# Kernel optimization log

Measured on AMD Instinct MI355X. Metric: run time of the kernel, lower is better.

Reference implementation:

```python
import jax, jax.numpy as jnp
import numpy as np

B, L, D_MODEL = 2, 1024, 512
N_LAYERS = 4
D_INNER = 2 * D_MODEL          # expand=2
D_STATE = 16
D_CONV = 4
DT_RANK = D_MODEL // 16        # ceil(512/16)=32
EPS = 1e-5


def layernorm(x, w, b):
    m = jnp.mean(x, axis=-1, keepdims=True)
    v = jnp.var(x, axis=-1, keepdims=True)
    return (x - m) * jax.lax.rsqrt(v + EPS) * w + b


def selective_scan(u, delta, A, Bm, Cm, Dp):
    # u, delta: [b,l,d]; Bm, Cm: [b,l,n]; A: [d,n]; Dp: [d]
    def step(h, inp):
        dt_t, b_t, c_t, u_t = inp            # [b,d],[b,n],[b,n],[b,d]
        dA = jnp.exp(dt_t[:, :, None] * A)   # [b,d,n]
        h = dA * h + (dt_t * u_t)[:, :, None] * b_t[:, None, :]
        y = jnp.einsum('bdn,bn->bd', h, c_t)
        return h, y

    b, l, d = u.shape
    n = A.shape[1]
    h0 = jnp.zeros((b, d, n), u.dtype)
    xs = (jnp.swapaxes(delta, 0, 1), jnp.swapaxes(Bm, 0, 1),
          jnp.swapaxes(Cm, 0, 1), jnp.swapaxes(u, 0, 1))
    _, ys = jax.lax.scan(step, h0, xs)       # ys: [l,b,d]
    return jnp.swapaxes(ys, 0, 1) + u * Dp


def mamba(x, in_w, conv_w, conv_b, xp_w, dtp_w, dtp_b, A_log, Dp, out_w):
    # x: [b,l,D_MODEL]
    xz = x @ in_w.T                          # [b,l,2*d_inner]
    xc, z = jnp.split(xz, 2, axis=-1)
    xc = jnp.swapaxes(xc, 1, 2)              # [b,d_inner,l]
    xc = jax.lax.conv_general_dilated(
        xc, conv_w[:, None, :], (1,), [(D_CONV - 1, 0)],
        feature_group_count=D_INNER,
        dimension_numbers=('NCH', 'OIH', 'NCH')) + conv_b[None, :, None]
    xc = jax.nn.silu(jnp.swapaxes(xc, 1, 2))  # [b,l,d_inner]
    x_dbl = xc @ xp_w.T                       # [b,l,dt_rank+2n]
    dt = x_dbl[..., :DT_RANK]
    Bm = x_dbl[..., DT_RANK:DT_RANK + D_STATE]
    Cm = x_dbl[..., DT_RANK + D_STATE:]
    dt = jax.nn.softplus(dt @ dtp_w.T + dtp_b)
    A = -jnp.exp(A_log)
    y = selective_scan(xc, dt, A, Bm, Cm, Dp)
    y = y * jax.nn.silu(z)
    return y @ out_w.T


def forward(x, in_proj_w, conv_w, conv_b, x_proj_w, dt_proj_w, dt_proj_b,
            A_log, D_param, out_proj_w, ln_w, ln_b, fnorm_w, fnorm_b):
    residual = None
    for i in range(in_proj_w.shape[0]):
        residual = x if residual is None else x + residual
        xn = layernorm(x, ln_w[i], ln_b[i])  # norm of incoming x (as in torch src)
        h1 = mamba(xn, in_proj_w[i, 0], conv_w[i, 0], conv_b[i, 0],
                   x_proj_w[i, 0], dt_proj_w[i, 0], dt_proj_b[i, 0],
                   A_log[i, 0], D_param[i, 0], out_proj_w[i, 0])
        h2 = mamba(jnp.flip(xn, axis=1), in_proj_w[i, 1], conv_w[i, 1],
                   conv_b[i, 1], x_proj_w[i, 1], dt_proj_w[i, 1],
                   dt_proj_b[i, 1], A_log[i, 1], D_param[i, 1],
                   out_proj_w[i, 1])
        x = h1 + h2                           # bi_add: NOT flipped back, faithful
    x = x + residual
    return layernorm(x, fnorm_w, fnorm_b)


def setup_inputs() -> dict:
    key = jax.random.key(0)
    ks = jax.random.split(key, 8)
    P2 = (N_LAYERS, 2)
    inp = {}
    inp['x'] = jax.random.normal(ks[0], (B, L, D_MODEL), jnp.float32)
    inp['in_proj_w'] = jax.random.normal(ks[1], P2 + (2 * D_INNER, D_MODEL), jnp.float32) * 0.02
    inp['conv_w'] = jax.random.normal(ks[2], P2 + (D_INNER, D_CONV), jnp.float32) * 0.1
    inp['conv_b'] = jnp.zeros(P2 + (D_INNER,), jnp.float32)
    inp['x_proj_w'] = jax.random.normal(ks[3], P2 + (DT_RANK + 2 * D_STATE, D_INNER), jnp.float32) * 0.02
    inp['dt_proj_w'] = jax.random.normal(ks[4], P2 + (D_INNER, DT_RANK), jnp.float32) * (DT_RANK ** -0.5)
    inp['dt_proj_b'] = jnp.full(P2 + (D_INNER,), float(np.log(np.expm1(0.01))), jnp.float32)
    inp['A_log'] = jnp.broadcast_to(jnp.log(jnp.arange(1, D_STATE + 1, dtype=jnp.float32)), P2 + (D_INNER, D_STATE)).copy()
    inp['D_param'] = jnp.ones(P2 + (D_INNER,), jnp.float32)
    inp['out_proj_w'] = jax.random.normal(ks[5], P2 + (D_MODEL, D_INNER), jnp.float32) * 0.02
    inp['ln_w'] = jnp.ones((N_LAYERS, D_MODEL), jnp.float32)
    inp['ln_b'] = jnp.zeros((N_LAYERS, D_MODEL), jnp.float32)
    inp['fnorm_w'] = jnp.ones((D_MODEL,), jnp.float32)
    inp['fnorm_b'] = jnp.zeros((D_MODEL,), jnp.float32)
    return inp


def reference(x, in_proj_w, conv_w, conv_b, x_proj_w, dt_proj_w, dt_proj_b,
              A_log, D_param, out_proj_w, ln_w, ln_b, fnorm_w, fnorm_b):
    return forward(x, in_proj_w, conv_w, conv_b, x_proj_w, dt_proj_w,
                   dt_proj_b, A_log, D_param, out_proj_w, ln_w, ln_b,
                   fnorm_w, fnorm_b)
```

## Files before the change

### kernel.cpp

```cpp
#include <hip/hip_runtime.h>
#include <hip/hip_bf16.h>
#include <type_traits>

#define B_   2
#define L_   1024
#define DM   512
#define DI   1024
#define DS   16
#define DTR  32
#define ROWS (B_*L_)
#define NCH  32
#define CHUNK (L_/NCH)

#define PO_CW    0
#define PO_CB    32768
#define PO_XPW   40960
#define PO_DTW   565248
#define PO_DTB   827392
#define PO_ALOG  835584
#define PO_DP    966656
#define PO_LNW   974848
#define PO_LNB   976896
#define PO_FNW   978944
#define PO_FNB   979456
#define PO_END   979968

#define N_WIN    (4*2097152)
#define N_WOUT   (4*1048576)
#define N_X      1048576

typedef __bf16 bf16x8 __attribute__((ext_vector_type(8)));
typedef float  f32x4  __attribute__((ext_vector_type(4)));
using bf16 = __hip_bfloat16;

__device__ __forceinline__ bf16x8 ld8(const bf16* p){
    return *reinterpret_cast<const bf16x8*>(p);
}
__device__ __forceinline__ float b2f(bf16 v){ return __bfloat162float(v); }

__device__ __forceinline__ unsigned pkbf2(float a, float b){
    bf16 ha = __float2bfloat16(a), hb = __float2bfloat16(b);
    unsigned short ua = *(unsigned short*)&ha, ub = *(unsigned short*)&hb;
    return (unsigned)ua | ((unsigned)ub << 16);
}
__device__ __forceinline__ float unpk_lo(unsigned v){
    unsigned x = v << 16; return __builtin_bit_cast(float, x);
}
__device__ __forceinline__ float unpk_hi(unsigned v){
    unsigned x = v & 0xffff0000u; return __builtin_bit_cast(float, x);
}

__device__ __forceinline__ void async_cp16(const void* g, void* s){
    __builtin_amdgcn_global_load_lds(
        (const __attribute__((address_space(1))) unsigned int*)g,
        (__attribute__((address_space(3))) unsigned int*)s, 16, 0, 0);
}

__global__ void detect_kernel(const void* Dp_raw, int* flag){
    *flag = (*(const unsigned int*)Dp_raw == 0x3F800000u) ? 1 : 0;
}

__device__ __forceinline__ bf16 cvload(const void* s, long o, int f){
    return f ? __float2bfloat16(((const float*)s)[o]) : ((const bf16*)s)[o];
}

__global__ void megacvt_kernel(const void* cw, const void* cb, const void* xpw,
                               const void* dtw, const void* dtb, const void* al,
                               const void* dp, const void* lnw, const void* lnb,
                               const void* fnw, const void* fnb,
                               const void* inw, const void* outw, const void* xin,
                               bf16* PP, bf16* WIN, bf16* WOUT,
                               float* X, float* R, const int* flag){
    long i = (long)blockIdx.x*256 + threadIdx.x;
    int f = *flag;
    if (i < PO_END){
        const void* s; long o;
        if      (i < PO_CB)   { s = cw;  o = i; }
        else if (i < PO_XPW)  { s = cb;  o = i - PO_CB; }
        else if (i < PO_DTW)  { s = xpw; o = i - PO_XPW; }
        else if (i < PO_DTB)  { s = dtw; o = i - PO_DTW; }
        else if (i < PO_ALOG) { s = dtb; o = i - PO_DTB; }
        else if (i < PO_DP)   { s = al;  o = i - PO_ALOG; }
        else if (i < PO_LNW)  { s = dp;  o = i - PO_DP; }
        else if (i < PO_LNB)  { s = lnw; o = i - PO_LNW; }
        else if (i < PO_FNW)  { s = lnb; o = i - PO_LNB; }
        else if (i < PO_FNB)  { s = fnw; o = i - PO_FNW; }
        else                  { s = fnb; o = i - PO_FNB; }
        PP[i] = cvload(s, o, f);
        return;
    }
    i -= PO_END;
    if (i < N_WIN){ WIN[i] = cvload(inw, i, f); return; }
    i -= N_WIN;
    if (i < N_WOUT){
        long l = i >> 20, r = i & 1048575;
        long n = r >> 11, dir = (r >> 10) & 1, d = r & 1023;
        WOUT[i] = cvload(outw, ((l*2 + dir)*512 + n)*1024 + d, f);
        return;
    }
    i -= N_WOUT;
    if (i < N_X){
        X[i] = f ? ((const float*)xin)[i] : b2f(((const bf16*)xin)[i]);
        R[i] = 0.f;
    }
}

__global__ void ln_kernel(const float* __restrict__ P, int nparts,
                          float* __restrict__ R,
                          const bf16* __restrict__ w, const bf16* __restrict__ b,
                          void* __restrict__ out, int mode, const int* flag){
    int row = blockIdx.x, lane = threadIdx.x;
    size_t base = (size_t)row*DM + lane*8;
    float v[8];
    *(float4*)&v[0] = *(const float4*)(P+base);
    *(float4*)&v[4] = *(const float4*)(P+base+4);
    for (int k=1; k<nparts; ++k){
        float4 a0 = *(const float4*)(P + (size_t)k*1048576 + base);
        float4 a1 = *(const float4*)(P + (size_t)k*1048576 + base + 4);
        v[0]+=a0.x; v[1]+=a0.y; v[2]+=a0.z; v[3]+=a0.w;
        v[4]+=a1.x; v[5]+=a1.y; v[6]+=a1.z; v[7]+=a1.w;
    }
    if (mode == 0){
        float4 r0 = *(const float4*)(R+base);
        float4 r1 = *(const float4*)(R+base+4);
        r0.x += v[0]; r0.y += v[1]; r0.z += v[2]; r0.w += v[3];
        r1.x += v[4]; r1.y += v[5]; r1.z += v[6]; r1.w += v[7];
        *(float4*)(R+base)   = r0;
        *(float4*)(R+base+4) = r1;
    } else {
        float4 r0 = *(const float4*)(R+base);
        float4 r1 = *(const float4*)(R+base+4);
        v[0]+=r0.x; v[1]+=r0.y; v[2]+=r0.z; v[3]+=r0.w;
        v[4]+=r1.x; v[5]+=r1.y; v[6]+=r1.z; v[7]+=r1.w;
    }
    float s=0.f, sq=0.f;
    #pragma unroll
    for (int j=0;j<8;++j){ s += v[j]; sq += v[j]*v[j]; }
    #pragma unroll
    for (int off=32; off>=1; off>>=1){
        s  += __shfl_xor(s,  off, 64);
        sq += __shfl_xor(sq, off, 64);
    }
    float mean = s*(1.f/DM);
    float var  = sq*(1.f/DM) - mean*mean;
    float rs   = rsqrtf(var + 1e-5f);
    bf16x8 wv = ld8(w + lane*8), bv = ld8(b + lane*8);
    float res[8];
    #pragma unroll
    for (int j=0;j<8;++j)
        res[j] = (v[j]-mean)*rs*(float)wv[j] + (float)bv[j];
    if (mode == 1 && *flag){
        float* of = (float*)out;
        *(float4*)(of+base)   = make_float4(res[0],res[1],res[2],res[3]);
        *(float4*)(of+base+4) = make_float4(res[4],res[5],res[6],res[7]);
    } else {
        union { bf16 h[8]; uint4 u; } o;
        #pragma unroll
        for (int j=0;j<8;++j) o.h[j] = __float2bfloat16(res[j]);
        *(uint4*)((bf16*)out + base) = o.u;
    }
}

template<int WM, int WN, int SK, typename CT>
__global__ __launch_bounds__(WM*WN*64)
void gemm_lds(const bf16* __restrict__ A, const bf16* __restrict__ W,
              CT* __restrict__ C, int K, int lda, int ldw, int ldc,
              int selTiles, long wSel){
    constexpr int BM = WM*64, BN = WN*64, T = WM*WN*64;
    constexpr int RA = (BM*4)/T, RB = (BN*4)/T;
    __shared__ __align__(16) bf16 sA[BM*32];
    __shared__ __align__(16) bf16 sB[BN*32];
    int tid = threadIdx.x;
    int mtile = blockIdx.y, ntile = blockIdx.x;
    if (mtile >= selTiles) W += wSel;
    int m0 = mtile*BM, n0 = ntile*BN;
    int kPer = K/SK, kBeg = blockIdx.z*kPer, kEnd = kBeg + kPer;
    if (SK > 1)
        C += (size_t)blockIdx.z * (size_t)(gridDim.y*BM) * (size_t)(gridDim.x*BN);
    int wave = tid>>6, lane = tid&63, quad = lane>>4, r = lane&15;
    int wrow = wave / WN, wcol = wave % WN;
    const bf16* Abase = A + (size_t)m0*lda;
    const bf16* Wbase = W + (size_t)n0*ldw;
    f32x4 acc[4][4] = {};
    for (int k0 = kBeg; k0 < kEnd; k0 += 32){
        #pragma unroll
        for (int rr=0; rr<RA; ++rr){
            int q = rr*T + tid;
            async_cp16(Abase + (size_t)(q>>2)*lda + k0 + (q&3)*8, &sA[q*8]);
        }
        #pragma unroll
        for (int rr=0; rr<RB; ++rr){
            int q = rr*T + tid;
            async_cp16(Wbase + (size_t)(q>>2)*ldw + k0 + (q&3)*8, &sB[q*8]);
        }
        __syncthreads();
        bf16x8 af[4], bw[4];
        #pragma unroll
        for (int mt=0; mt<4; ++mt)
            af[mt] = *(const bf16x8*)&sA[(wrow*64 + mt*16 + r)*32 + quad*8];
        #pragma unroll
        for (int nt=0; nt<4; ++nt)
            bw[nt] = *(const bf16x8*)&sB[(wcol*64 + nt*16 + r)*32 + quad*8];
        #pragma unroll
        for (int mt=0; mt<4; ++mt)
            #pragma unroll
            for (int nt=0; nt<4; ++nt)
                acc[mt][nt] = __builtin_amdgcn_mfma_f32_16x16x32_bf16(
                    af[mt], bw[nt], acc[mt][nt], 0,0,0);
        __syncthreads();
    }
    #pragma unroll
    for (int mt=0; mt<4; ++mt){
        #pragma unroll
        for (int nt=0; nt<4; ++nt){
            int col = n0 + wcol*64 + nt*16 + r;
            #pragma unroll
            for (int ri=0; ri<4; ++ri){
                int row = m0 + wrow*64 + mt*16 + quad*4 + ri;
                size_t idx = (size_t)row*ldc + col;
                if constexpr (std::is_same<CT, bf16>::value)
                    C[idx] = __float2bfloat16(acc[mt][nt][ri]);
                else
                    C[idx] = acc[mt][nt][ri];
            }
        }
    }
}

__global__ void reduce_xd(const float* __restrict__ P, float* __restrict__ XD){
    int i = blockIdx.x*256 + threadIdx.x;
    float s = 0.f;
    #pragma unroll
    for (int k=0;k<8;++k) s += P[k*262144 + i];
    int j = i & 63, grow = i >> 6, dir = grow >> 11, row = grow & 2047;
    XD[row*128 + dir*64 + j] = s;
}

__global__ void conv_kernel(const bf16* __restrict__ XZ, const bf16* __restrict__ cw,
                            const bf16* __restrict__ cb, const bf16* __restrict__ Dp,
                            bf16* __restrict__ XC, unsigned* __restrict__ GU){
    int id  = blockIdx.x*256 + threadIdx.x;
    int d   = id & (DI-1);
    int t   = (id >> 10) & (L_-1);
    int b   = (id >> 20) & 1;
    int dir = id >> 21;
    float wv[4];
    #pragma unroll
    for (int k=0;k<4;++k) wv[k] = b2f(cw[((size_t)dir*DI + d)*4 + k]);
    float acc = b2f(cb[dir*DI + d]);
    #pragma unroll
    for (int k=0;k<4;++k){
        int tau = t - 3 + k;
        if (tau >= 0){
            int sig = dir ? (L_-1-tau) : tau;
            acc += wv[k] * b2f(XZ[((size_t)(b*L_ + sig))*4096 + dir*2048 + d]);
        }
    }
    float u = acc * (1.f/(1.f + __expf(-acc)));
    size_t idx = ((size_t)dir*ROWS + (size_t)b*L_ + t)*DI + d;
    XC[idx] = __float2bfloat16(u);
    int sig3 = dir ? (L_-1-t) : t;
    float zv = b2f(XZ[((size_t)(b*L_ + sig3))*4096 + dir*2048 + 1024 + d]);
    float g  = zv*(1.f/(1.f + __expf(-zv)));
    float Dv = b2f(Dp[dir*DI + d]);
    GU[idx] = pkbf2(g, u*Dv*g);
}

__global__ void dtproj_kernel(const float* __restrict__ XD, const bf16* __restrict__ dtw,
                              const bf16* __restrict__ dtb, const bf16* __restrict__ XC,
                              unsigned* __restrict__ DTW){
    int id  = blockIdx.x*256 + threadIdx.x;
    int d   = id & (DI-1);
    int row = (id >> 10) & (ROWS-1);
    int dir = id >> 21;
    const float* xr = XD + (size_t)row*128 + dir*64;
    const bf16*  wp = dtw + ((size_t)dir*DI + d)*DTR;
    float acc = b2f(dtb[dir*DI + d]);
    #pragma unroll
    for (int kk=0;kk<4;++kk){
        bf16x8 wv = ld8(wp + kk*8);
        #pragma unroll
        for (int j=0;j<8;++j) acc += xr[kk*8+j]*(float)wv[j];
    }
    float sp = acc > 20.f ? acc : log1pf(__expf(acc));
    size_t idx = ((size_t)dir*ROWS + row)*DI + d;
    float u = b2f(XC[idx]);
    DTW[idx] = pkbf2(sp, sp*u);
}

template<int PHASE>
__global__ __launch_bounds__(256)
void scan_phase(const unsigned* __restrict__ DTW, const unsigned* __restrict__ GU,
                const float* __restrict__ XD, const bf16* __restrict__ Al,
                float* __restrict__ SP, float* __restrict__ SH,
                bf16* __restrict__ Y){
    int dirb = blockIdx.z, dir = dirb >> 1, b = dirb & 1;
    int c    = blockIdx.y;
    int d0   = blockIdx.x*128;
    int tid  = threadIdx.x;
    int dl   = tid >> 1, nh = tid & 1;
    int d    = d0 + dl;

    __shared__ __align__(16) unsigned sDTW[CHUNK*128];
    __shared__ __align__(16) float    sBC[CHUNK][32];
    __shared__ __align__(16) unsigned sGU[(PHASE==3)?CHUNK*128:4];

    const unsigned* DTWb = DTW + ((size_t)dir*ROWS + b*L_ + c*CHUNK)*DI + d0;
    #pragma unroll
    for (int it=0; it<4; ++it){
        int q = it*256 + tid;
        int t = q >> 5, c4 = q & 31;
        async_cp16(DTWb + (size_t)t*DI + c4*4, &sDTW[q*4]);
    }
    if (PHASE == 3){
        const unsigned* GUb = GU + ((size_t)dir*ROWS + b*L_ + c*CHUNK)*DI + d0;
        #pragma unroll
        for (int it=0; it<4; ++it){
            int q = it*256 + tid;
            int t = q >> 5, c4 = q & 31;
            async_cp16(GUb + (size_t)t*DI + c4*4, &sGU[q*4]);
        }
    }
    {
        int t = tid >> 3, j = tid & 7;
        async_cp16(XD + ((size_t)(b*L_) + c*CHUNK + t)*128 + dir*64 + 32 + j*4,
                   &sBC[t][j*4]);
    }

    float An[8];
    {
        const bf16* ap = Al + ((size_t)dir*DI + d)*DS + nh*8;
        bf16x8 av = ld8(ap);
        #pragma unroll
        for (int j=0;j<8;++j) An[j] = -__expf((float)av[j]);
    }

    float h[8], pr[8];
    #pragma unroll
    for (int j=0;j<8;++j){ h[j]=0.f; pr[j]=1.f; }
    size_t so = ((size_t)(dirb*NCH + c)*DI + d)*DS + nh*8;
    if (PHASE == 3){
        for (int cc=0; cc<c; ++cc){
            size_t o = ((size_t)(dirb*NCH + cc)*DI + d)*DS + nh*8;
            f32x4 p0 = *(const f32x4*)&SP[o];
            f32x4 p1 = *(const f32x4*)&SP[o+4];
            f32x4 h0 = *(const f32x4*)&SH[o];
            f32x4 h1 = *(const f32x4*)&SH[o+4];
            #pragma unroll
            for (int j=0;j<4;++j){
                h[j]   = p0[j]*h[j]   + h0[j];
                h[4+j] = p1[j]*h[4+j] + h1[j];
            }
        }
    }
    __syncthreads();

    bf16* Yp = Y + ((size_t)b*L_ + c*CHUNK)*2048 + dir*DI + d;

    #pragma unroll 4
    for (int tl=0; tl<CHUNK; ++tl){
        unsigned dw = sDTW[tl*128 + dl];
        float dtv = unpk_lo(dw), wv = unpk_hi(dw);
        const float* Bp = &sBC[tl][nh*8];
        float y = 0.f;
        #pragma unroll
        for (int j=0;j<8;++j){
            float dA = __expf(dtv*An[j]);
            h[j] = dA*h[j] + wv*Bp[j];
            if (PHASE == 1) pr[j] *= dA;
            else            y += h[j]*Bp[16+j];
        }
        if (PHASE == 3){
            y += __shfl_xor(y, 1, 64);
            if (nh == 0){
                unsigned gu = sGU[tl*128 + dl];
                Yp[(size_t)tl*2048] = __float2bfloat16(y*unpk_lo(gu) + unpk_hi(gu));
            }
        }
    }
    if (PHASE == 1){
        *(f32x4*)&SP[so]   = *(f32x4*)&pr[0];
        *(f32x4*)&SP[so+4] = *(f32x4*)&pr[4];
        *(f32x4*)&SH[so]   = *(f32x4*)&h[0];
        *(f32x4*)&SH[so+4] = *(f32x4*)&h[4];
    }
}

extern "C" void kernel_launch(void* const* d_in, const int* in_sizes, int n_in,
                              void* d_out, int out_size, void* d_ws, size_t ws_size,
                              hipStream_t stream){
    const void* x_raw    = d_in[0];
    const void* inw_raw  = d_in[1];
    const void* convw_raw= d_in[2];
    const void* convb_raw= d_in[3];
    const void* xpw_raw  = d_in[4];
    const void* dtw_raw  = d_in[5];
    const void* dtb_raw  = d_in[6];
    const void* alog_raw = d_in[7];
    const void* dp_raw   = d_in[8];
    const void* outw_raw = d_in[9];
    const void* lnw_raw  = d_in[10];
    const void* lnb_raw  = d_in[11];
    const void* fnw_raw  = d_in[12];
    const void* fnb_raw  = d_in[13];

    char* ws = (char*)d_ws;
    float*    X   = (float*)   (ws + 0);
    float*    R   = (float*)   (ws + 4194304);
    bf16*     XN  = (bf16*)    (ws + 8388608);
    bf16*     XZ  = (bf16*)    (ws + 10485760);
    bf16*     XC  = (bf16*)    (ws + 27262976);
    float*    XD  = (float*)   (ws + 35651584);
    unsigned* DTW = (unsigned*)(ws + 36700160);
    unsigned* GU  = (unsigned*)(ws + 52428800);
    bf16*     Y   = (bf16*)    (ws + 68157440);
    float*    SP  = (float*)   (ws + 76546048);
    float*    SH  = (float*)   (ws + 84934656);
    bf16*     PP  = (bf16*)    (ws + 93323264);
    bf16*     WIN = (bf16*)    (ws + 95420416);
    bf16*     WOUT= (bf16*)    (ws + 112197632);
    float*    PX  = (float*)   (ws + 120586240);
    float*    PO  = (float*)   (ws + 128974848);
    int*      FLAG= (int*)     (ws + 145752064);

    detect_kernel<<<1,1,0,stream>>>(dp_raw, FLAG);
    {
        long total = (long)PO_END + N_WIN + N_WOUT + N_X;
        int blocks = (int)((total + 255)/256);
        megacvt_kernel<<<blocks,256,0,stream>>>(
            convw_raw, convb_raw, xpw_raw, dtw_raw, dtb_raw, alog_raw, dp_raw,
            lnw_raw, lnb_raw, fnw_raw, fnb_raw, inw_raw, outw_raw, x_raw,
            PP, WIN, WOUT, X, R, FLAG);
    }

    for (int l=0; l<4; ++l){
        ln_kernel<<<ROWS,64,0,stream>>>(l==0 ? X : PO, l==0 ? 1 : 4, R,
                                        PP+PO_LNW+l*DM, PP+PO_LNB+l*DM, XN, 0, FLAG);

        gemm_lds<2,2,1,bf16><<<dim3(32,16,1),256,0,stream>>>(
            XN, WIN + (size_t)l*2097152, XZ, 512, 512, 512, 4096, 1<<30, 0);

        conv_kernel<<<16384,256,0,stream>>>(XZ, PP+PO_CW + (size_t)l*2*DI*4,
                                            PP+PO_CB + l*2*DI, PP+PO_DP + l*2*DI,
                                            XC, GU);

        gemm_lds<2,1,8,float><<<dim3(1,32,8),128,0,stream>>>(
            XC, PP+PO_XPW + (size_t)l*2*64*DI, PX, 1024, 1024, 1024, 64,
            16, (long)64*DI);
        reduce_xd<<<1024,256,0,stream>>>(PX, XD);

        dtproj_kernel<<<16384,256,0,stream>>>(XD, PP+PO_DTW + (size_t)l*2*DI*DTR,
                                              PP+PO_DTB + l*2*DI, XC, DTW);

        scan_phase<1><<<dim3(DI/128,NCH,4),256,0,stream>>>(
            DTW, GU, XD, PP+PO_ALOG + (size_t)l*2*DI*DS, SP, SH, Y);
        scan_phase<3><<<dim3(DI/128,NCH,4),256,0,stream>>>(
            DTW, GU, XD, PP+PO_ALOG + (size_t)l*2*DI*DS, SP, SH, Y);

        gemm_lds<2,2,4,float><<<dim3(4,16,4),256,0,stream>>>(
            Y, WOUT + (size_t)l*1048576, PO, 2048, 2048, 2048, 512, 1<<30, 0);
    }

    ln_kernel<<<ROWS,64,0,stream>>>(PO, 4, R, PP+PO_FNW, PP+PO_FNB, d_out, 1, FLAG);
}
```

Before: 771.2 us.

## Widen GEMM K-tile, fuse split-K reduce into dtproj, vectorize conv and scan

The GEMM K-tile becomes a template parameter, set to 64, so each barrier pair covers twice the MFMA work and the loop makes fewer trips. The separate reduce_xd kernel is removed: dtproj now sums the split-K partials itself into shared memory and writes only the B/C part of XD, which saves one launch and one pass through memory. The conv kernel handles two channels per thread with packed loads and stores. The scan loop reads B and C as float4 vectors. The cost is that each dtproj block recomputes the dt-rank reduction, and LDS usage grows with the larger K tile.

```diff
diff --git a/kernel.cpp b/kernel.cpp
--- a/kernel.cpp
+++ b/kernel.cpp
@@ -161,15 +161,16 @@
     }
 }
 
-template<int WM, int WN, int SK, typename CT>
+template<int WM, int WN, int SK, int BK, typename CT>
 __global__ __launch_bounds__(WM*WN*64)
 void gemm_lds(const bf16* __restrict__ A, const bf16* __restrict__ W,
               CT* __restrict__ C, int K, int lda, int ldw, int ldc,
               int selTiles, long wSel){
     constexpr int BM = WM*64, BN = WN*64, T = WM*WN*64;
-    constexpr int RA = (BM*4)/T, RB = (BN*4)/T;
-    __shared__ __align__(16) bf16 sA[BM*32];
-    __shared__ __align__(16) bf16 sB[BN*32];
+    constexpr int KC = BK/8;
+    constexpr int RA = (BM*KC)/T, RB = (BN*KC)/T;
+    __shared__ __align__(16) bf16 sA[BM*BK];
+    __shared__ __align__(16) bf16 sB[BN*BK];
     int tid = threadIdx.x;
     int mtile = blockIdx.y, ntile = blockIdx.x;
     if (mtile >= selTiles) W += wSel;
@@ -182,31 +183,36 @@
     const bf16* Abase = A + (size_t)m0*lda;
     const bf16* Wbase = W + (size_t)n0*ldw;
     f32x4 acc[4][4] = {};
-    for (int k0 = kBeg; k0 < kEnd; k0 += 32){
+    for (int k0 = kBeg; k0 < kEnd; k0 += BK){
         #pragma unroll
         for (int rr=0; rr<RA; ++rr){
             int q = rr*T + tid;
-            async_cp16(Abase + (size_t)(q>>2)*lda + k0 + (q&3)*8, &sA[q*8]);
+            int row = q/KC, cp = q%KC;
+            async_cp16(Abase + (size_t)row*lda + k0 + cp*8, &sA[q*8]);
         }
         #pragma unroll
         for (int rr=0; rr<RB; ++rr){
             int q = rr*T + tid;
-            async_cp16(Wbase + (size_t)(q>>2)*ldw + k0 + (q&3)*8, &sB[q*8]);
+            int row = q/KC, cp = q%KC;
+            async_cp16(Wbase + (size_t)row*ldw + k0 + cp*8, &sB[q*8]);
         }
         __syncthreads();
-        bf16x8 af[4], bw[4];
-        #pragma unroll
-        for (int mt=0; mt<4; ++mt)
-            af[mt] = *(const bf16x8*)&sA[(wrow*64 + mt*16 + r)*32 + quad*8];
-        #pragma unroll
-        for (int nt=0; nt<4; ++nt)
-            bw[nt] = *(const bf16x8*)&sB[(wcol*64 + nt*16 + r)*32 + quad*8];
-        #pragma unroll
-        for (int mt=0; mt<4; ++mt)
+        #pragma unroll
+        for (int ko=0; ko<BK; ko+=32){
+            bf16x8 af[4], bw[4];
+            #pragma unroll
+            for (int mt=0; mt<4; ++mt)
+                af[mt] = *(const bf16x8*)&sA[(wrow*64 + mt*16 + r)*BK + ko + quad*8];
             #pragma unroll
             for (int nt=0; nt<4; ++nt)
-                acc[mt][nt] = __builtin_amdgcn_mfma_f32_16x16x32_bf16(
-                    af[mt], bw[nt], acc[mt][nt], 0,0,0);
+                bw[nt] = *(const bf16x8*)&sB[(wcol*64 + nt*16 + r)*BK + ko + quad*8];
+            #pragma unroll
+            for (int mt=0; mt<4; ++mt)
+                #pragma unroll
+                for (int nt=0; nt<4; ++nt)
+                    acc[mt][nt] = __builtin_amdgcn_mfma_f32_16x16x32_bf16(
+                        af[mt], bw[nt], acc[mt][nt], 0,0,0);
+        }
         __syncthreads();
     }
     #pragma unroll
@@ -227,60 +233,71 @@
     }
 }
 
-__global__ void reduce_xd(const float* __restrict__ P, float* __restrict__ XD){
-    int i = blockIdx.x*256 + threadIdx.x;
-    float s = 0.f;
-    #pragma unroll
-    for (int k=0;k<8;++k) s += P[k*262144 + i];
-    int j = i & 63, grow = i >> 6, dir = grow >> 11, row = grow & 2047;
-    XD[row*128 + dir*64 + j] = s;
-}
-
 __global__ void conv_kernel(const bf16* __restrict__ XZ, const bf16* __restrict__ cw,
                             const bf16* __restrict__ cb, const bf16* __restrict__ Dp,
                             bf16* __restrict__ XC, unsigned* __restrict__ GU){
     int id  = blockIdx.x*256 + threadIdx.x;
-    int d   = id & (DI-1);
-    int t   = (id >> 10) & (L_-1);
-    int b   = (id >> 20) & 1;
-    int dir = id >> 21;
-    float wv[4];
-    #pragma unroll
-    for (int k=0;k<4;++k) wv[k] = b2f(cw[((size_t)dir*DI + d)*4 + k]);
-    float acc = b2f(cb[dir*DI + d]);
+    int d   = (id & 511) * 2;
+    int t   = (id >> 9) & (L_-1);
+    int b   = (id >> 19) & 1;
+    int dir = id >> 20;
+    bf16x8 wv8 = ld8(cw + ((size_t)dir*DI + d)*4);
+    unsigned pcb = *(const unsigned*)&cb[dir*DI + d];
+    float acc0 = unpk_lo(pcb), acc1 = unpk_hi(pcb);
     #pragma unroll
     for (int k=0;k<4;++k){
         int tau = t - 3 + k;
         if (tau >= 0){
             int sig = dir ? (L_-1-tau) : tau;
-            acc += wv[k] * b2f(XZ[((size_t)(b*L_ + sig))*4096 + dir*2048 + d]);
-        }
-    }
-    float u = acc * (1.f/(1.f + __expf(-acc)));
+            unsigned pz = *(const unsigned*)&XZ[((size_t)(b*L_ + sig))*4096 + dir*2048 + d];
+            acc0 += (float)wv8[k]   * unpk_lo(pz);
+            acc1 += (float)wv8[4+k] * unpk_hi(pz);
+        }
+    }
+    float u0 = acc0 * (1.f/(1.f + __expf(-acc0)));
+    float u1 = acc1 * (1.f/(1.f + __expf(-acc1)));
     size_t idx = ((size_t)dir*ROWS + (size_t)b*L_ + t)*DI + d;
-    XC[idx] = __float2bfloat16(u);
+    *(unsigned*)&XC[idx] = pkbf2(u0, u1);
     int sig3 = dir ? (L_-1-t) : t;
-    float zv = b2f(XZ[((size_t)(b*L_ + sig3))*4096 + dir*2048 + 1024 + d]);
-    float g  = zv*(1.f/(1.f + __expf(-zv)));
-    float Dv = b2f(Dp[dir*DI + d]);
-    GU[idx] = pkbf2(g, u*Dv*g);
-}
-
-__global__ void dtproj_kernel(const float* __restrict__ XD, const bf16* __restrict__ dtw,
+    unsigned pzz = *(const unsigned*)&XZ[((size_t)(b*L_ + sig3))*4096 + dir*2048 + 1024 + d];
+    float z0 = unpk_lo(pzz), z1 = unpk_hi(pzz);
+    float g0 = z0*(1.f/(1.f + __expf(-z0)));
+    float g1 = z1*(1.f/(1.f + __expf(-z1)));
+    unsigned pdv = *(const unsigned*)&Dp[dir*DI + d];
+    *(uint2*)&GU[idx] = make_uint2(pkbf2(g0, u0*unpk_lo(pdv)*g0),
+                                   pkbf2(g1, u1*unpk_hi(pdv)*g1));
+}
+
+__global__ void dtproj_kernel(const float* __restrict__ PX, const bf16* __restrict__ dtw,
                               const bf16* __restrict__ dtb, const bf16* __restrict__ XC,
-                              unsigned* __restrict__ DTW){
+                              unsigned* __restrict__ DTW, float* __restrict__ XD){
     int id  = blockIdx.x*256 + threadIdx.x;
     int d   = id & (DI-1);
     int row = (id >> 10) & (ROWS-1);
     int dir = id >> 21;
-    const float* xr = XD + (size_t)row*128 + dir*64;
-    const bf16*  wp = dtw + ((size_t)dir*DI + d)*DTR;
+    int tid = threadIdx.x;
+    int grow = dir*2048 + row;
+    __shared__ float sXR[32];
+    if (tid < 32){
+        float s = 0.f;
+        #pragma unroll
+        for (int k=0;k<8;++k) s += PX[(size_t)k*262144 + (size_t)grow*64 + tid];
+        sXR[tid] = s;
+    } else if (tid < 64 && ((id >> 8) & 3) == 0){
+        int j = tid - 32;
+        float s = 0.f;
+        #pragma unroll
+        for (int k=0;k<8;++k) s += PX[(size_t)k*262144 + (size_t)grow*64 + 32 + j];
+        XD[(size_t)row*128 + dir*64 + 32 + j] = s;
+    }
+    __syncthreads();
+    const bf16* wp = dtw + ((size_t)dir*DI + d)*DTR;
     float acc = b2f(dtb[dir*DI + d]);
     #pragma unroll
     for (int kk=0;kk<4;++kk){
         bf16x8 wv = ld8(wp + kk*8);
         #pragma unroll
-        for (int j=0;j<8;++j) acc += xr[kk*8+j]*(float)wv[j];
+        for (int j=0;j<8;++j) acc += sXR[kk*8+j]*(float)wv[j];
     }
     float sp = acc > 20.f ? acc : log1pf(__expf(acc));
     size_t idx = ((size_t)dir*ROWS + row)*DI + d;
@@ -361,14 +378,19 @@
     for (int tl=0; tl<CHUNK; ++tl){
         unsigned dw = sDTW[tl*128 + dl];
         float dtv = unpk_lo(dw), wv = unpk_hi(dw);
-        const float* Bp = &sBC[tl][nh*8];
+        f32x4 Bv0 = *(const f32x4*)&sBC[tl][nh*8];
+        f32x4 Bv1 = *(const f32x4*)&sBC[tl][nh*8+4];
+        f32x4 Cv0 = *(const f32x4*)&sBC[tl][16+nh*8];
+        f32x4 Cv1 = *(const f32x4*)&sBC[tl][16+nh*8+4];
         float y = 0.f;
         #pragma unroll
-        for (int j=0;j<8;++j){
-            float dA = __expf(dtv*An[j]);
-            h[j] = dA*h[j] + wv*Bp[j];
-            if (PHASE == 1) pr[j] *= dA;
-            else            y += h[j]*Bp[16+j];
+        for (int j=0;j<4;++j){
+            float dA0 = __expf(dtv*An[j]);
+            float dA1 = __expf(dtv*An[4+j]);
+            h[j]   = dA0*h[j]   + wv*Bv0[j];
+            h[4+j] = dA1*h[4+j] + wv*Bv1[j];
+            if (PHASE == 1){ pr[j] *= dA0; pr[4+j] *= dA1; }
+            else { y += h[j]*Cv0[j]; y += h[4+j]*Cv1[j]; }
         }
         if (PHASE == 3){
             y += __shfl_xor(y, 1, 64);
@@ -437,27 +459,26 @@
         ln_kernel<<<ROWS,64,0,stream>>>(l==0 ? X : PO, l==0 ? 1 : 4, R,
                                         PP+PO_LNW+l*DM, PP+PO_LNB+l*DM, XN, 0, FLAG);
 
-        gemm_lds<2,2,1,bf16><<<dim3(32,16,1),256,0,stream>>>(
+        gemm_lds<2,2,1,64,bf16><<<dim3(32,16,1),256,0,stream>>>(
             XN, WIN + (size_t)l*2097152, XZ, 512, 512, 512, 4096, 1<<30, 0);
 
-        conv_kernel<<<16384,256,0,stream>>>(XZ, PP+PO_CW + (size_t)l*2*DI*4,
-                                            PP+PO_CB + l*2*DI, PP+PO_DP + l*2*DI,
-                                            XC, GU);
-
-        gemm_lds<2,1,8,float><<<dim3(1,32,8),128,0,stream>>>(
+        conv_kernel<<<8192,256,0,stream>>>(XZ, PP+PO_CW + (size_t)l*2*DI*4,
+                                           PP+PO_CB + l*2*DI, PP+PO_DP + l*2*DI,
+                                           XC, GU);
+
+        gemm_lds<2,1,8,64,float><<<dim3(1,32,8),128,0,stream>>>(
             XC, PP+PO_XPW + (size_t)l*2*64*DI, PX, 1024, 1024, 1024, 64,
             16, (long)64*DI);
-        reduce_xd<<<1024,256,0,stream>>>(PX, XD);
-
-        dtproj_kernel<<<16384,256,0,stream>>>(XD, PP+PO_DTW + (size_t)l*2*DI*DTR,
-                                              PP+PO_DTB + l*2*DI, XC, DTW);
+
+        dtproj_kernel<<<16384,256,0,stream>>>(PX, PP+PO_DTW + (size_t)l*2*DI*DTR,
+                                              PP+PO_DTB + l*2*DI, XC, DTW, XD);
 
         scan_phase<1><<<dim3(DI/128,NCH,4),256,0,stream>>>(
             DTW, GU, XD, PP+PO_ALOG + (size_t)l*2*DI*DS, SP, SH, Y);
         scan_phase<3><<<dim3(DI/128,NCH,4),256,0,stream>>>(
             DTW, GU, XD, PP+PO_ALOG + (size_t)l*2*DI*DS, SP, SH, Y);
 
-        gemm_lds<2,2,4,float><<<dim3(4,16,4),256,0,stream>>>(
+        gemm_lds<2,2,4,64,float><<<dim3(4,16,4),256,0,stream>>>(
             Y, WOUT + (size_t)l*1048576, PO, 2048, 2048, 2048, 512, 1<<30, 0);
     }
 
```

Measured after the change: 701.8 us. 9.0% less time.
